# Optimization experiments

Measured on AMD Instinct MI355X. Metric: run time of the kernel, lower is better.

Reference implementation:

```python
import jax, jax.numpy as jnp
import numpy as np

B, N, E, OD, RD, ED, H = 4, 2048, 8192, 3, 4, 4, 8


def _linear(x, W, b):
    return x @ W + b


def _mlp_rel(x, p):
    # RelationalModel: Lin-ELU-Lin-ELU-Lin-ELU-Lin
    h = jax.nn.elu(_linear(x, p[0], p[1]))
    h = jax.nn.elu(_linear(h, p[2], p[3]))
    h = jax.nn.elu(_linear(h, p[4], p[5]))
    return _linear(h, p[6], p[7])


def _mlp_obj(x, p):
    # ObjectModel: Lin-ELU-Lin-ELU-Lin
    h = jax.nn.elu(_linear(x, p[0], p[1]))
    h = jax.nn.elu(_linear(h, p[2], p[3]))
    return _linear(h, p[4], p[5])


def setup_inputs() -> dict:
    key = jax.random.key(0)
    ks = jax.random.split(key, 24)
    X = jax.random.normal(ks[0], (B, OD, N), jnp.float32)
    Ra = jax.random.normal(ks[1], (B, E, RD), jnp.float32)
    # one-hot incidence matrices (receiver / sender), as in the torch repo
    ro_idx = jax.random.randint(ks[2], (B, E), 0, N)
    ri_idx = jax.random.randint(ks[3], (B, E), 0, N)
    Ro = jax.nn.one_hot(ro_idx, N, dtype=jnp.float32)
    Ri = jax.nn.one_hot(ri_idx, N, dtype=jnp.float32)

    def w(k, i, o):
        return jax.random.normal(k, (i, o), jnp.float32) * (1.0 / np.sqrt(i))

    def b(k, o):
        return jax.random.normal(k, (o,), jnp.float32) * 0.01

    m_in = 2 * OD + RD  # 10
    d = {
        "X": X, "Ra": Ra, "Ro": Ro, "Ri": Ri,
        # phi_R1: m_in -> H -> H -> H -> ED
        "r1W1": w(ks[4], m_in, H), "r1b1": b(ks[5], H),
        "r1W2": w(ks[6], H, H), "r1b2": b(ks[7], H),
        "r1W3": w(ks[8], H, H), "r1b3": b(ks[9], H),
        "r1W4": w(ks[10], H, ED), "r1b4": b(ks[11], ED),
        # phi_R2: m_in -> H -> H -> H -> 1
        "r2W1": w(ks[12], m_in, H), "r2b1": b(ks[13], H),
        "r2W2": w(ks[14], H, H), "r2b2": b(ks[15], H),
        "r2W3": w(ks[16], H, H), "r2b3": b(ks[17], H),
        "r2W4": w(ks[18], H, 1), "r2b4": b(ks[19], 1),
        # phi_O: OD+ED -> H -> H -> 3
        "oW1": w(ks[20], OD + ED, H), "ob1": b(ks[21], H),
        "oW2": w(ks[22], H, H), "ob2": b(ks[23], H),
        "oW3": w(jax.random.fold_in(key, 99), H, 3),
        "ob3": jnp.zeros((3,), jnp.float32),
    }
    return d


def reference(X, Ra, Ro, Ri,
              r1W1, r1b1, r1W2, r1b2, r1W3, r1b3, r1W4, r1b4,
              r2W1, r2b1, r2W2, r2b2, r2W3, r2b3, r2W4, r2b4,
              oW1, ob1, oW2, ob2, oW3, ob3):
    r1 = (r1W1, r1b1, r1W2, r1b2, r1W3, r1b3, r1W4, r1b4)
    r2 = (r2W1, r2b1, r2W2, r2b2, r2W3, r2b3, r2W4, r2b4)
    po = (oW1, ob1, oW2, ob2, oW3, ob3)

    Xt = jnp.swapaxes(X, 1, 2)          # [B, N, OD]
    Xi = jnp.einsum('ben,bnd->bed', Ro, Xt)   # receiver gather [B,E,OD]
    Xo = jnp.einsum('ben,bnd->bed', Ri, Xt)   # sender gather   [B,E,OD]
    m1 = jnp.concatenate([Xi, Xo, Ra], axis=2)  # [B,E,2*OD+RD]
    Eff = _mlp_rel(m1, r1)              # [B,E,ED]
    A = jnp.einsum('ben,bed->bnd', Ri, Eff)     # scatter-add to nodes [B,N,ED]
    C = jnp.concatenate([Xt, A], axis=2)        # [B,N,OD+ED]
    X_tilde = _mlp_obj(C, po)           # [B,N,3]
    Xi_t = jnp.einsum('ben,bnd->bed', Ri, X_tilde)
    Xo_t = jnp.einsum('ben,bnd->bed', Ro, X_tilde)
    m2 = jnp.concatenate([Xi_t, Xo_t, Eff], axis=2)  # [B,E,6+ED]
    W = jax.nn.sigmoid(_mlp_rel(m2, r2))  # [B,E,1]
    return W
```

## Files before the change

### kernel.cpp

```cpp
#include <hip/hip_runtime.h>
#include <hip/hip_bf16.h>
#include <cstdint>

#define NBATCH 4
#define NNODE  2048
#define NEDGE  8192
#define ETOT   (NBATCH * NEDGE)
#define NTOT   (NBATCH * NNODE)

typedef uint32_t u32x4 __attribute__((ext_vector_type(4)));

__device__ __forceinline__ float elu(float x) {
    return x > 0.0f ? x : expm1f(x);
}

__global__ void in_idx_kernel(const u32x4* __restrict__ Ro,
                              const u32x4* __restrict__ Ri,
                              int* __restrict__ ro_idx,
                              int* __restrict__ ri_idx,
                              float* __restrict__ A, int a_elems) {
    const int gtid = blockIdx.x * blockDim.x + threadIdx.x;
    if (gtid < a_elems) A[gtid] = 0.0f;

    const int wid  = gtid >> 6;
    const int lane = threadIdx.x & 63;
    const int nrows = 2 * ETOT;
    if (wid >= nrows) return;

    const bool second = (wid >= ETOT);
    const int  row    = second ? wid - ETOT : wid;
    const u32x4* __restrict__ src = (second ? Ri : Ro) + (size_t)row * (NNODE / 4);
    int* __restrict__ dst = second ? ri_idx : ro_idx;

    #pragma unroll
    for (int c = 0; c < NNODE / 256; ++c) {
        const u32x4 v = src[c * 64 + lane];
        const uint32_t o = v.x | v.y | v.z | v.w;
        const unsigned long long found = __ballot(o != 0u);
        if (found) {
            if (o) {
                const int base = c * 256 + lane * 4;
                if      (v.x) dst[row] = base;
                else if (v.y) dst[row] = base + 1;
                else if (v.z) dst[row] = base + 2;
                else          dst[row] = base + 3;
            }
            break;
        }
    }
}

__global__ void in_edge1_kernel(const float* __restrict__ X,
                                const float* __restrict__ Ra,
                                const int* __restrict__ ro_idx,
                                const int* __restrict__ ri_idx,
                                const float* __restrict__ W1, const float* __restrict__ b1,
                                const float* __restrict__ W2, const float* __restrict__ b2,
                                const float* __restrict__ W3, const float* __restrict__ b3,
                                const float* __restrict__ W4, const float* __restrict__ b4,
                                float* __restrict__ Eff,
                                float* __restrict__ A) {
    __shared__ float sW1[80], sb1[8], sW2[64], sb2[8], sW3[64], sb3[8], sW4[32], sb4[4];
    const int t = threadIdx.x, bs = blockDim.x;
    for (int i = t; i < 80; i += bs) sW1[i] = W1[i];
    for (int i = t; i < 8;  i += bs) sb1[i] = b1[i];
    for (int i = t; i < 64; i += bs) sW2[i] = W2[i];
    for (int i = t; i < 8;  i += bs) sb2[i] = b2[i];
    for (int i = t; i < 64; i += bs) sW3[i] = W3[i];
    for (int i = t; i < 8;  i += bs) sb3[i] = b3[i];
    for (int i = t; i < 32; i += bs) sW4[i] = W4[i];
    for (int i = t; i < 4;  i += bs) sb4[i] = b4[i];
    __syncthreads();

    const int e = blockIdx.x * blockDim.x + threadIdx.x;
    if (e >= ETOT) return;
    const int b  = e >> 13;
    const int ro = ro_idx[e] & (NNODE - 1);
    const int ri = ri_idx[e] & (NNODE - 1);

    float x[10];
    const float* Xb = X + (long)b * 3 * NNODE;
    #pragma unroll
    for (int d = 0; d < 3; ++d) x[d]     = Xb[d * NNODE + ro];
    #pragma unroll
    for (int d = 0; d < 3; ++d) x[3 + d] = Xb[d * NNODE + ri];
    const float4 ra = ((const float4*)Ra)[e];
    x[6] = ra.x; x[7] = ra.y; x[8] = ra.z; x[9] = ra.w;

    float h1[8], h2[8], h3[8];
    #pragma unroll
    for (int j = 0; j < 8; ++j) {
        float s = sb1[j];
        #pragma unroll
        for (int i = 0; i < 10; ++i) s += x[i] * sW1[i * 8 + j];
        h1[j] = elu(s);
    }
    #pragma unroll
    for (int j = 0; j < 8; ++j) {
        float s = sb2[j];
        #pragma unroll
        for (int i = 0; i < 8; ++i) s += h1[i] * sW2[i * 8 + j];
        h2[j] = elu(s);
    }
    #pragma unroll
    for (int j = 0; j < 8; ++j) {
        float s = sb3[j];
        #pragma unroll
        for (int i = 0; i < 8; ++i) s += h2[i] * sW3[i * 8 + j];
        h3[j] = elu(s);
    }
    float* Arow = A + ((long)(b * NNODE + ri)) * 4;
    float4 eff;
    float* effp = (float*)&eff;
    #pragma unroll
    for (int j = 0; j < 4; ++j) {
        float s = sb4[j];
        #pragma unroll
        for (int i = 0; i < 8; ++i) s += h3[i] * sW4[i * 4 + j];
        effp[j] = s;
        atomicAdd(&Arow[j], s);
    }
    ((float4*)Eff)[e] = eff;
}

__global__ void in_node_kernel(const float* __restrict__ X,
                               const float* __restrict__ A,
                               const float* __restrict__ W1, const float* __restrict__ b1,
                               const float* __restrict__ W2, const float* __restrict__ b2,
                               const float* __restrict__ W3, const float* __restrict__ b3,
                               float* __restrict__ Xtil) {
    __shared__ float sW1[56], sb1[8], sW2[64], sb2[8], sW3[24], sb3[3];
    const int t = threadIdx.x, bs = blockDim.x;
    for (int i = t; i < 56; i += bs) sW1[i] = W1[i];
    for (int i = t; i < 8;  i += bs) sb1[i] = b1[i];
    for (int i = t; i < 64; i += bs) sW2[i] = W2[i];
    for (int i = t; i < 8;  i += bs) sb2[i] = b2[i];
    for (int i = t; i < 24; i += bs) sW3[i] = W3[i];
    for (int i = t; i < 3;  i += bs) sb3[i] = b3[i];
    __syncthreads();

    const int n = blockIdx.x * blockDim.x + threadIdx.x;
    if (n >= NTOT) return;
    const int b  = n >> 11;
    const int nn = n & (NNODE - 1);

    float c[7];
    const float* Xb = X + (long)b * 3 * NNODE;
    #pragma unroll
    for (int d = 0; d < 3; ++d) c[d] = Xb[d * NNODE + nn];
    const float4 a4 = ((const float4*)A)[n];
    c[3] = a4.x; c[4] = a4.y; c[5] = a4.z; c[6] = a4.w;

    float h1[8], h2[8];
    #pragma unroll
    for (int j = 0; j < 8; ++j) {
        float s = sb1[j];
        #pragma unroll
        for (int i = 0; i < 7; ++i) s += c[i] * sW1[i * 8 + j];
        h1[j] = elu(s);
    }
    #pragma unroll
    for (int j = 0; j < 8; ++j) {
        float s = sb2[j];
        #pragma unroll
        for (int i = 0; i < 8; ++i) s += h1[i] * sW2[i * 8 + j];
        h2[j] = elu(s);
    }
    #pragma unroll
    for (int j = 0; j < 3; ++j) {
        float s = sb3[j];
        #pragma unroll
        for (int i = 0; i < 8; ++i) s += h2[i] * sW3[i * 3 + j];
        Xtil[(long)n * 3 + j] = s;
    }
}

__global__ void in_edge2_kernel(const float* __restrict__ Xtil,
                                const float* __restrict__ Eff,
                                const int* __restrict__ ro_idx,
                                const int* __restrict__ ri_idx,
                                const float* __restrict__ W1, const float* __restrict__ b1,
                                const float* __restrict__ W2, const float* __restrict__ b2,
                                const float* __restrict__ W3, const float* __restrict__ b3,
                                const float* __restrict__ W4, const float* __restrict__ b4,
                                float* __restrict__ out) {
    __shared__ float sW1[80], sb1[8], sW2[64], sb2[8], sW3[64], sb3[8], sW4[8], sb4[1];
    const int t = threadIdx.x, bs = blockDim.x;
    for (int i = t; i < 80; i += bs) sW1[i] = W1[i];
    for (int i = t; i < 8;  i += bs) sb1[i] = b1[i];
    for (int i = t; i < 64; i += bs) sW2[i] = W2[i];
    for (int i = t; i < 8;  i += bs) sb2[i] = b2[i];
    for (int i = t; i < 64; i += bs) sW3[i] = W3[i];
    for (int i = t; i < 8;  i += bs) sb3[i] = b3[i];
    for (int i = t; i < 8;  i += bs) sW4[i] = W4[i];
    for (int i = t; i < 1;  i += bs) sb4[i] = b4[i];
    __syncthreads();

    const int e = blockIdx.x * blockDim.x + threadIdx.x;
    if (e >= ETOT) return;
    const int b  = e >> 13;
    const int ro = ro_idx[e] & (NNODE - 1);
    const int ri = ri_idx[e] & (NNODE - 1);

    float x[10];
    const float* Xb = Xtil + (long)b * NNODE * 3;
    #pragma unroll
    for (int d = 0; d < 3; ++d) x[d]     = Xb[(long)ri * 3 + d];
    #pragma unroll
    for (int d = 0; d < 3; ++d) x[3 + d] = Xb[(long)ro * 3 + d];
    const float4 ef = ((const float4*)Eff)[e];
    x[6] = ef.x; x[7] = ef.y; x[8] = ef.z; x[9] = ef.w;

    float h1[8], h2[8], h3[8];
    #pragma unroll
    for (int j = 0; j < 8; ++j) {
        float s = sb1[j];
        #pragma unroll
        for (int i = 0; i < 10; ++i) s += x[i] * sW1[i * 8 + j];
        h1[j] = elu(s);
    }
    #pragma unroll
    for (int j = 0; j < 8; ++j) {
        float s = sb2[j];
        #pragma unroll
        for (int i = 0; i < 8; ++i) s += h1[i] * sW2[i * 8 + j];
        h2[j] = elu(s);
    }
    #pragma unroll
    for (int j = 0; j < 8; ++j) {
        float s = sb3[j];
        #pragma unroll
        for (int i = 0; i < 8; ++i) s += h2[i] * sW3[i * 8 + j];
        h3[j] = elu(s);
    }
    float s = sb4[0];
    #pragma unroll
    for (int i = 0; i < 8; ++i) s += h3[i] * sW4[i];
    out[e] = 1.0f / (1.0f + expf(-s));
}

extern "C" void kernel_launch(void* const* d_in, const int* in_sizes, int n_in,
                              void* d_out, int out_size, void* d_ws, size_t ws_size,
                              hipStream_t stream) {
    const float* X  = (const float*)d_in[0];
    const float* Ra = (const float*)d_in[1];
    const float* Ro = (const float*)d_in[2];
    const float* Ri = (const float*)d_in[3];
    const float* r1W1 = (const float*)d_in[4];  const float* r1b1 = (const float*)d_in[5];
    const float* r1W2 = (const float*)d_in[6];  const float* r1b2 = (const float*)d_in[7];
    const float* r1W3 = (const float*)d_in[8];  const float* r1b3 = (const float*)d_in[9];
    const float* r1W4 = (const float*)d_in[10]; const float* r1b4 = (const float*)d_in[11];
    const float* r2W1 = (const float*)d_in[12]; const float* r2b1 = (const float*)d_in[13];
    const float* r2W2 = (const float*)d_in[14]; const float* r2b2 = (const float*)d_in[15];
    const float* r2W3 = (const float*)d_in[16]; const float* r2b3 = (const float*)d_in[17];
    const float* r2W4 = (const float*)d_in[18]; const float* r2b4 = (const float*)d_in[19];
    const float* oW1  = (const float*)d_in[20]; const float* ob1  = (const float*)d_in[21];
    const float* oW2  = (const float*)d_in[22]; const float* ob2  = (const float*)d_in[23];
    const float* oW3  = (const float*)d_in[24]; const float* ob3  = (const float*)d_in[25];

    char* ws = (char*)d_ws;
    int*   ro_idx = (int*)(ws + 0);
    int*   ri_idx = (int*)(ws + 131072);
    float* Eff    = (float*)(ws + 262144);
    float* A      = (float*)(ws + 786432);
    float* Xtil   = (float*)(ws + 917504);

    in_idx_kernel<<<(2 * ETOT * 64) / 256, 256, 0, stream>>>(
        (const u32x4*)Ro, (const u32x4*)Ri, ro_idx, ri_idx, A, NTOT * 4 );

    in_edge1_kernel<<<ETOT / 256, 256, 0, stream>>>(X, Ra, ro_idx, ri_idx,
                                                    r1W1, r1b1, r1W2, r1b2, r1W3, r1b3, r1W4, r1b4,
                                                    Eff, A);

    in_node_kernel<<<NTOT / 256, 256, 0, stream>>>(X, A,
                                                   oW1, ob1, oW2, ob2, oW3, ob3,
                                                   Xtil);

    in_edge2_kernel<<<ETOT / 256, 256, 0, stream>>>(Xtil, Eff, ro_idx, ri_idx,
                                                    r2W1, r2b1, r2W2, r2b2, r2W3, r2b3, r2W4, r2b4,
                                                    (float*)d_out);
}
```

Before: 80.18 us.

## Fuse one-hot index scan into edge MLP kernel with wave-per-edge layout

Merges the one-hot index extraction kernel into the first edge MLP kernel, so one wavefront handles one edge. The wavefront scans the Ro and Ri rows together with nontemporal loads and broadcasts the found indices with a shuffle. It then computes the 8-wide hidden layers across lanes using shuffles instead of running the whole MLP in each thread. This removes a kernel launch and the index round-trip through memory, and zeroing A moves to hipMemsetAsync. In exchange, most lanes sit idle during the MLP, and the added memset call may carry its own overhead.

```diff
diff --git a/kernel.cpp b/kernel.cpp
--- a/kernel.cpp
+++ b/kernel.cpp
@@ -14,52 +14,18 @@
     return x > 0.0f ? x : expm1f(x);
 }
 
-__global__ void in_idx_kernel(const u32x4* __restrict__ Ro,
-                              const u32x4* __restrict__ Ri,
-                              int* __restrict__ ro_idx,
-                              int* __restrict__ ri_idx,
-                              float* __restrict__ A, int a_elems) {
-    const int gtid = blockIdx.x * blockDim.x + threadIdx.x;
-    if (gtid < a_elems) A[gtid] = 0.0f;
-
-    const int wid  = gtid >> 6;
-    const int lane = threadIdx.x & 63;
-    const int nrows = 2 * ETOT;
-    if (wid >= nrows) return;
-
-    const bool second = (wid >= ETOT);
-    const int  row    = second ? wid - ETOT : wid;
-    const u32x4* __restrict__ src = (second ? Ri : Ro) + (size_t)row * (NNODE / 4);
-    int* __restrict__ dst = second ? ri_idx : ro_idx;
-
-    #pragma unroll
-    for (int c = 0; c < NNODE / 256; ++c) {
-        const u32x4 v = src[c * 64 + lane];
-        const uint32_t o = v.x | v.y | v.z | v.w;
-        const unsigned long long found = __ballot(o != 0u);
-        if (found) {
-            if (o) {
-                const int base = c * 256 + lane * 4;
-                if      (v.x) dst[row] = base;
-                else if (v.y) dst[row] = base + 1;
-                else if (v.z) dst[row] = base + 2;
-                else          dst[row] = base + 3;
-            }
-            break;
-        }
-    }
-}
-
-__global__ void in_edge1_kernel(const float* __restrict__ X,
-                                const float* __restrict__ Ra,
-                                const int* __restrict__ ro_idx,
-                                const int* __restrict__ ri_idx,
-                                const float* __restrict__ W1, const float* __restrict__ b1,
-                                const float* __restrict__ W2, const float* __restrict__ b2,
-                                const float* __restrict__ W3, const float* __restrict__ b3,
-                                const float* __restrict__ W4, const float* __restrict__ b4,
-                                float* __restrict__ Eff,
-                                float* __restrict__ A) {
+__global__ __launch_bounds__(256, 6)
+void in_scan_edge1_kernel(const u32x4* __restrict__ Ro,
+                          const u32x4* __restrict__ Ri,
+                          const float* __restrict__ X,
+                          const float* __restrict__ Ra,
+                          const float* __restrict__ W1, const float* __restrict__ b1,
+                          const float* __restrict__ W2, const float* __restrict__ b2,
+                          const float* __restrict__ W3, const float* __restrict__ b3,
+                          const float* __restrict__ W4, const float* __restrict__ b4,
+                          int* __restrict__ ro_idx, int* __restrict__ ri_idx,
+                          float* __restrict__ Eff,
+                          float* __restrict__ A) {
     __shared__ float sW1[80], sb1[8], sW2[64], sb2[8], sW3[64], sb3[8], sW4[32], sb4[4];
     const int t = threadIdx.x, bs = blockDim.x;
     for (int i = t; i < 80; i += bs) sW1[i] = W1[i];
@@ -72,55 +38,85 @@
     for (int i = t; i < 4;  i += bs) sb4[i] = b4[i];
     __syncthreads();
 
-    const int e = blockIdx.x * blockDim.x + threadIdx.x;
-    if (e >= ETOT) return;
+    const int gtid = blockIdx.x * blockDim.x + threadIdx.x;
+    const int e    = gtid >> 6;
+    const int lane = threadIdx.x & 63;
+
+    const u32x4* __restrict__ pa = Ro + (size_t)e * (NNODE / 4);
+    const u32x4* __restrict__ pb = Ri + (size_t)e * (NNODE / 4);
+
+    int ro = -1, ri = -1;
+    int ca = 0, cb = 0;
+    while (true) {
+        u32x4 va, vb;
+        const bool la = (ro < 0), lb = (ri < 0);
+        if (la) va = __builtin_nontemporal_load(&pa[ca * 64 + lane]);
+        if (lb) vb = __builtin_nontemporal_load(&pb[cb * 64 + lane]);
+        if (la) {
+            const uint32_t o = va.x | va.y | va.z | va.w;
+            const unsigned long long m = __ballot(o != 0u);
+            if (m) {
+                const int base = ca * 256 + lane * 4;
+                int my;
+                if      (va.x) my = base;
+                else if (va.y) my = base + 1;
+                else if (va.z) my = base + 2;
+                else           my = base + 3;
+                ro = __shfl(my, (int)(__ffsll(m) - 1));
+            } else if (++ca >= NNODE / 256) ro = 0;
+        }
+        if (lb) {
+            const uint32_t o = vb.x | vb.y | vb.z | vb.w;
+            const unsigned long long m = __ballot(o != 0u);
+            if (m) {
+                const int base = cb * 256 + lane * 4;
+                int my;
+                if      (vb.x) my = base;
+                else if (vb.y) my = base + 1;
+                else if (vb.z) my = base + 2;
+                else           my = base + 3;
+                ri = __shfl(my, (int)(__ffsll(m) - 1));
+            } else if (++cb >= NNODE / 256) ri = 0;
+        }
+        if (ro >= 0 && ri >= 0) break;
+    }
+    if (lane == 0) { ro_idx[e] = ro; ri_idx[e] = ri; }
+
     const int b  = e >> 13;
-    const int ro = ro_idx[e] & (NNODE - 1);
-    const int ri = ri_idx[e] & (NNODE - 1);
-
+    const int jj = lane & 7;
+    const float* Xb = X + (long)b * 3 * NNODE;
     float x[10];
-    const float* Xb = X + (long)b * 3 * NNODE;
     #pragma unroll
     for (int d = 0; d < 3; ++d) x[d]     = Xb[d * NNODE + ro];
     #pragma unroll
     for (int d = 0; d < 3; ++d) x[3 + d] = Xb[d * NNODE + ri];
-    const float4 ra = ((const float4*)Ra)[e];
-    x[6] = ra.x; x[7] = ra.y; x[8] = ra.z; x[9] = ra.w;
-
-    float h1[8], h2[8], h3[8];
-    #pragma unroll
-    for (int j = 0; j < 8; ++j) {
-        float s = sb1[j];
-        #pragma unroll
-        for (int i = 0; i < 10; ++i) s += x[i] * sW1[i * 8 + j];
-        h1[j] = elu(s);
-    }
-    #pragma unroll
-    for (int j = 0; j < 8; ++j) {
-        float s = sb2[j];
-        #pragma unroll
-        for (int i = 0; i < 8; ++i) s += h1[i] * sW2[i * 8 + j];
-        h2[j] = elu(s);
-    }
-    #pragma unroll
-    for (int j = 0; j < 8; ++j) {
-        float s = sb3[j];
-        #pragma unroll
-        for (int i = 0; i < 8; ++i) s += h2[i] * sW3[i * 8 + j];
-        h3[j] = elu(s);
-    }
-    float* Arow = A + ((long)(b * NNODE + ri)) * 4;
-    float4 eff;
-    float* effp = (float*)&eff;
-    #pragma unroll
-    for (int j = 0; j < 4; ++j) {
-        float s = sb4[j];
-        #pragma unroll
-        for (int i = 0; i < 8; ++i) s += h3[i] * sW4[i * 4 + j];
-        effp[j] = s;
-        atomicAdd(&Arow[j], s);
-    }
-    ((float4*)Eff)[e] = eff;
+    const float4 ra4 = ((const float4*)Ra)[e];
+    x[6] = ra4.x; x[7] = ra4.y; x[8] = ra4.z; x[9] = ra4.w;
+
+    float s1 = sb1[jj];
+    #pragma unroll
+    for (int i = 0; i < 10; ++i) s1 += x[i] * sW1[i * 8 + jj];
+    const float h1 = elu(s1);
+
+    float s2 = sb2[jj];
+    #pragma unroll
+    for (int i = 0; i < 8; ++i) s2 += __shfl(h1, i) * sW2[i * 8 + jj];
+    const float h2 = elu(s2);
+
+    float s3 = sb3[jj];
+    #pragma unroll
+    for (int i = 0; i < 8; ++i) s3 += __shfl(h2, i) * sW3[i * 8 + jj];
+    const float h3 = elu(s3);
+
+    const int j4 = lane & 3;
+    float s4 = sb4[j4];
+    #pragma unroll
+    for (int i = 0; i < 8; ++i) s4 += __shfl(h3, i) * sW4[i * 4 + j4];
+
+    if (lane < 4) {
+        Eff[(long)e * 4 + lane] = s4;
+        atomicAdd(&A[((long)(b * NNODE + ri)) * 4 + lane], s4);
+    }
 }
 
 __global__ void in_node_kernel(const float* __restrict__ X,
@@ -265,12 +261,12 @@
     float* A      = (float*)(ws + 786432);
     float* Xtil   = (float*)(ws + 917504);
 
-    in_idx_kernel<<<(2 * ETOT * 64) / 256, 256, 0, stream>>>(
-        (const u32x4*)Ro, (const u32x4*)Ri, ro_idx, ri_idx, A, NTOT * 4 );
-
-    in_edge1_kernel<<<ETOT / 256, 256, 0, stream>>>(X, Ra, ro_idx, ri_idx,
-                                                    r1W1, r1b1, r1W2, r1b2, r1W3, r1b3, r1W4, r1b4,
-                                                    Eff, A);
+    hipMemsetAsync(A, 0, (size_t)NTOT * 4 * sizeof(float), stream);
+
+    in_scan_edge1_kernel<<<ETOT * 64 / 256, 256, 0, stream>>>(
+        (const u32x4*)Ro, (const u32x4*)Ri, X, Ra,
+        r1W1, r1b1, r1W2, r1b2, r1W3, r1b3, r1W4, r1b4,
+        ro_idx, ri_idx, Eff, A);
 
     in_node_kernel<<<NTOT / 256, 256, 0, stream>>>(X, A,
                                                    oW1, ob1, oW2, ob2, oW3, ob3,
```

Result: slower. 87.67 us (+9.3%).
